# Optimization experiments

Hardware: AMD Instinct MI355X
Metric: run time of the kernel (lower is better)

The kernel has to match this reference:

```python
import jax, jax.numpy as jnp
import numpy as np

B, H, Q, D = 2, 8, 4096, 32
GH, GW = 32, 32  # key grid height/width


def setup_inputs() -> dict:
    key = jax.random.key(0)
    k1, k2, k3, k4 = jax.random.split(key, 4)
    queries = jax.random.normal(k1, (B, H, Q, D), dtype=jnp.float32)
    keys = jax.random.normal(k2, (B, H, GH, GW, D), dtype=jnp.float32)
    pos = jax.random.randint(k3, (B, Q, 2), 0, GH)  # integer (y, x) grid position of each query
    rel_bias = jax.random.normal(k4, (H, 2 * GH - 1, 2 * GW - 1), dtype=jnp.float32)
    return {"queries": queries, "keys": keys, "pos": pos, "rel_bias": rel_bias}


def reference(queries, keys, pos, rel_bias):
    # queries: [B,H,Q,D]; keys: [B,H,GH,GW,D]; pos: [B,Q,2] int; rel_bias: [H,2GH-1,2GW-1]
    b, h, q, d = queries.shape
    gh, gw = keys.shape[2], keys.shape[3]
    scale = 1.0 / jnp.sqrt(jnp.asarray(d, queries.dtype))
    # attention scores against every grid cell: [B,H,Q,GH,GW]
    scores = jnp.einsum('bhqd,bhijd->bhqij', queries, keys) * scale
    # relative offset indices into the bias table
    rel_y = jnp.arange(gh)[None, None, :] - pos[..., 0][..., None] + (gh - 1)  # [B,Q,GH]
    rel_x = jnp.arange(gw)[None, None, :] - pos[..., 1][..., None] + (gw - 1)  # [B,Q,GW]
    # gather per-head bias: [H,B,Q,GH,GW] -> [B,H,Q,GH,GW]
    bias = rel_bias[:, rel_y[:, :, :, None], rel_x[:, :, None, :]]
    bias = jnp.transpose(bias, (1, 0, 2, 3, 4))
    logits = scores + bias
    attn = jax.nn.softmax(logits.reshape(b, h, q, gh * gw), axis=-1)
    return attn.reshape(b, h, q, gh, gw)
```

## Files before the change

### kernel.cpp

```cpp
#include <hip/hip_runtime.h>

namespace {
constexpr int B_ = 2, H_ = 8, Q_ = 4096, D_ = 32;
constexpr int NPOS = 1024;
constexpr int NB = 63;
constexpr int NT = 512;
constexpr int QCHUNK = 128;
constexpr float SCALE = 0.17677669529663687f;
constexpr float LOG2E = 1.4426950408889634f;
constexpr float C1 = SCALE * LOG2E;
}

typedef __attribute__((ext_vector_type(8))) short short8;
typedef __attribute__((ext_vector_type(4))) float float4v;

__device__ __forceinline__ unsigned short f2bf(float f) {
  unsigned u = __float_as_uint(f);
  u += 0x7fffu + ((u >> 16) & 1u);
  return (unsigned short)(u >> 16);
}

__device__ __forceinline__ float fexp2(float x) {
#if defined(__has_builtin)
#if __has_builtin(__builtin_amdgcn_exp2f)
  return __builtin_amdgcn_exp2f(x);
#else
  return exp2f(x);
#endif
#else
  return exp2f(x);
#endif
}

__device__ __forceinline__ float frcp(float x) {
#if defined(__has_builtin)
#if __has_builtin(__builtin_amdgcn_rcpf)
  return __builtin_amdgcn_rcpf(x);
#else
  return 1.0f / x;
#endif
#else
  return 1.0f / x;
#endif
}

__global__ __launch_bounds__(NT, 4)
void rga_kernel(const float* __restrict__ queries,
                const float* __restrict__ keys,
                const int*   __restrict__ pos,
                const float* __restrict__ rel_bias,
                float* __restrict__ out) {
  __shared__ __align__(16) unsigned short klds[NPOS * D_];

  const int t    = threadIdx.x;
  const int lane = t & 63;
  const int w    = t >> 6;
  const int m    = lane & 15;
  const int quad = lane >> 4;
  const int h  = blockIdx.y;
  const int b  = blockIdx.z;
  const int bh = b * H_ + h;
  const int q0 = blockIdx.x * QCHUNK;

  {
    const float4* src = (const float4*)(keys + (size_t)bh * (NPOS * D_));
    #pragma unroll
    for (int i = 0; i < (NPOS * D_ / 4) / NT; ++i) {
      float4 v = src[i * NT + t];
      unsigned lo = (unsigned)f2bf(v.x) | ((unsigned)f2bf(v.y) << 16);
      unsigned hi = (unsigned)f2bf(v.z) | ((unsigned)f2bf(v.w) << 16);
      ((uint2*)klds)[i * NT + t] = make_uint2(lo, hi);
    }
  }
  __syncthreads();

  const int qrow = q0 + w * 16 + m;

  short8 afrag;
  {
    const float* qp = queries + ((size_t)(bh * Q_) + qrow) * D_ + quad * 8;
    float4 x = *(const float4*)(qp);
    float4 y = *(const float4*)(qp + 4);
    afrag[0] = (short)f2bf(x.x); afrag[1] = (short)f2bf(x.y);
    afrag[2] = (short)f2bf(x.z); afrag[3] = (short)f2bf(x.w);
    afrag[4] = (short)f2bf(y.x); afrag[5] = (short)f2bf(y.y);
    afrag[6] = (short)f2bf(y.z); afrag[7] = (short)f2bf(y.w);
  }

  const float* bbase;
  {
    int2 p = *(const int2*)(pos + ((size_t)b * Q_ + qrow) * 2);
    bbase = rel_bias + (size_t)h * (NB * NB)
          + (31 - p.x) * NB + (31 - p.y) + quad * 4;
  }

  const unsigned short* kbase = klds + m * D_ + quad * 8;

  float sum = 0.f;
  #pragma unroll
  for (int n = 0; n < NPOS / 16; ++n) {
    const short8 kf = *(const short8*)(kbase + n * 512);
    float4v acc = __builtin_amdgcn_mfma_f32_16x16x32_bf16(
        kf, afrag, (float4v){0.f, 0.f, 0.f, 0.f}, 0, 0, 0);
    float4v bv;
    __builtin_memcpy(&bv, bbase + (n >> 1) * NB + ((n & 1) << 4), 16);
    float e0 = fexp2(acc[0] * C1 + bv[0] * LOG2E);
    float e1 = fexp2(acc[1] * C1 + bv[1] * LOG2E);
    float e2 = fexp2(acc[2] * C1 + bv[2] * LOG2E);
    float e3 = fexp2(acc[3] * C1 + bv[3] * LOG2E);
    sum += (e0 + e1) + (e2 + e3);
  }
  sum += __shfl_xor(sum, 16, 64);
  sum += __shfl_xor(sum, 32, 64);
  const float rinv = frcp(sum);

  float* orow = out + ((size_t)(bh * Q_) + qrow) * NPOS + quad * 4;
  #pragma unroll
  for (int n = 0; n < NPOS / 16; ++n) {
    const short8 kf = *(const short8*)(kbase + n * 512);
    float4v acc = __builtin_amdgcn_mfma_f32_16x16x32_bf16(
        kf, afrag, (float4v){0.f, 0.f, 0.f, 0.f}, 0, 0, 0);
    float4v bv;
    __builtin_memcpy(&bv, bbase + (n >> 1) * NB + ((n & 1) << 4), 16);
    float4v ev;
    ev[0] = fexp2(acc[0] * C1 + bv[0] * LOG2E) * rinv;
    ev[1] = fexp2(acc[1] * C1 + bv[1] * LOG2E) * rinv;
    ev[2] = fexp2(acc[2] * C1 + bv[2] * LOG2E) * rinv;
    ev[3] = fexp2(acc[3] * C1 + bv[3] * LOG2E) * rinv;
    __builtin_nontemporal_store(ev, (float4v*)(orow + n * 16));
  }
}

extern "C" void kernel_launch(void* const* d_in, const int* in_sizes, int n_in,
                              void* d_out, int out_size, void* d_ws, size_t ws_size,
                              hipStream_t stream) {
  const float* queries  = (const float*)d_in[0];
  const float* keys     = (const float*)d_in[1];
  const int*   pos      = (const int*)d_in[2];
  const float* rel_bias = (const float*)d_in[3];
  float* out = (float*)d_out;

  dim3 grid(Q_ / QCHUNK, H_, B_);
  dim3 block(NT);
  hipLaunchKernelGGL(rga_kernel, grid, block, 0, stream,
                     queries, keys, pos, rel_bias, out);
}
```

Before: 339.5 us.

## Split key columns across waves, cache exps as bf16 in registers, swizzle LDS

Each block now covers 64 queries with 16 waves. Every group of 4 waves splits the 1024 key positions so that each wave handles 256 columns, and the partial row sums are combined through shared memory. The exponentials from the first pass are kept in registers as truncated bf16 pairs. The second pass only rescales and stores them instead of redoing the MFMA, the bias loads and exp2. The key LDS layout gets an XOR swizzle so reads avoid bank conflicts. The cost is an extra block barrier, fewer queries per block for the same key staging work, and a loss of output precision from truncating to bf16.

```diff
diff --git a/kernel.cpp b/kernel.cpp
--- a/kernel.cpp
+++ b/kernel.cpp
@@ -4,8 +4,8 @@
 constexpr int B_ = 2, H_ = 8, Q_ = 4096, D_ = 32;
 constexpr int NPOS = 1024;
 constexpr int NB = 63;
-constexpr int NT = 512;
-constexpr int QCHUNK = 128;
+constexpr int NT = 1024;
+constexpr int QCHUNK = 64;
 constexpr float SCALE = 0.17677669529663687f;
 constexpr float LOG2E = 1.4426950408889634f;
 constexpr float C1 = SCALE * LOG2E;
@@ -18,6 +18,10 @@
   unsigned u = __float_as_uint(f);
   u += 0x7fffu + ((u >> 16) & 1u);
   return (unsigned short)(u >> 16);
+}
+
+__device__ __forceinline__ unsigned pack2bf(float a, float b) {
+  return (unsigned)f2bf(a) | ((unsigned)f2bf(b) << 16);
 }
 
 __device__ __forceinline__ float fexp2(float x) {
@@ -44,37 +48,59 @@
 #endif
 }
 
+__device__ __forceinline__ unsigned pack_hi16(unsigned hi_from, unsigned lo_from) {
+#if defined(__has_builtin)
+#if __has_builtin(__builtin_amdgcn_perm)
+  return __builtin_amdgcn_perm(hi_from, lo_from, 0x07060302u);
+#else
+  return (lo_from >> 16) | (hi_from & 0xffff0000u);
+#endif
+#else
+  return (lo_from >> 16) | (hi_from & 0xffff0000u);
+#endif
+}
+
 __global__ __launch_bounds__(NT, 4)
 void rga_kernel(const float* __restrict__ queries,
                 const float* __restrict__ keys,
                 const int*   __restrict__ pos,
                 const float* __restrict__ rel_bias,
                 float* __restrict__ out) {
-  __shared__ __align__(16) unsigned short klds[NPOS * D_];
+  __shared__ __align__(16) unsigned char klds[NPOS * 64];
 
   const int t    = threadIdx.x;
   const int lane = t & 63;
   const int w    = t >> 6;
   const int m    = lane & 15;
   const int quad = lane >> 4;
+  const int rg   = w >> 2;
+  const int cw   = w & 3;
   const int h  = blockIdx.y;
   const int b  = blockIdx.z;
   const int bh = b * H_ + h;
   const int q0 = blockIdx.x * QCHUNK;
 
   {
-    const float4* src = (const float4*)(keys + (size_t)bh * (NPOS * D_));
+    const float* src = keys + (size_t)bh * (NPOS * D_);
     #pragma unroll
-    for (int i = 0; i < (NPOS * D_ / 4) / NT; ++i) {
-      float4 v = src[i * NT + t];
-      unsigned lo = (unsigned)f2bf(v.x) | ((unsigned)f2bf(v.y) << 16);
-      unsigned hi = (unsigned)f2bf(v.z) | ((unsigned)f2bf(v.w) << 16);
-      ((uint2*)klds)[i * NT + t] = make_uint2(lo, hi);
+    for (int i = 0; i < 4; ++i) {
+      const int c = i * NT + t;
+      const int p = c >> 2;
+      const int cq = c & 3;
+      float4 x = *(const float4*)(src + (size_t)c * 8);
+      float4 y = *(const float4*)(src + (size_t)c * 8 + 4);
+      uint4 v;
+      v.x = pack2bf(x.x, x.y);
+      v.y = pack2bf(x.z, x.w);
+      v.z = pack2bf(y.x, y.y);
+      v.w = pack2bf(y.z, y.w);
+      const int pq = cq ^ (p & 3) ^ ((p >> 2) & 3);
+      *(uint4*)(klds + (size_t)p * 64 + pq * 16) = v;
     }
   }
   __syncthreads();
 
-  const int qrow = q0 + w * 16 + m;
+  const int qrow = q0 + rg * 16 + m;
 
   short8 afrag;
   {
@@ -94,12 +120,15 @@
           + (31 - p.x) * NB + (31 - p.y) + quad * 4;
   }
 
-  const unsigned short* kbase = klds + m * D_ + quad * 8;
+  const unsigned char* kbase =
+      klds + (size_t)m * 64 + ((quad ^ (m & 3) ^ ((m >> 2) & 3)) << 4);
 
   float sum = 0.f;
+  unsigned Epk[32];
   #pragma unroll
-  for (int n = 0; n < NPOS / 16; ++n) {
-    const short8 kf = *(const short8*)(kbase + n * 512);
+  for (int k = 0; k < 16; ++k) {
+    const int n = cw * 16 + k;
+    const short8 kf = *(const short8*)(kbase + n * 1024);
     float4v acc = __builtin_amdgcn_mfma_f32_16x16x32_bf16(
         kf, afrag, (float4v){0.f, 0.f, 0.f, 0.f}, 0, 0, 0);
     float4v bv;
@@ -109,24 +138,31 @@
     float e2 = fexp2(acc[2] * C1 + bv[2] * LOG2E);
     float e3 = fexp2(acc[3] * C1 + bv[3] * LOG2E);
     sum += (e0 + e1) + (e2 + e3);
+    Epk[2 * k]     = pack_hi16(__float_as_uint(e1), __float_as_uint(e0));
+    Epk[2 * k + 1] = pack_hi16(__float_as_uint(e3), __float_as_uint(e2));
   }
+
   sum += __shfl_xor(sum, 16, 64);
   sum += __shfl_xor(sum, 32, 64);
-  const float rinv = frcp(sum);
+
+  __syncthreads();
+  float* slds = (float*)klds;
+  if (lane < 16) slds[w * 16 + m] = sum;
+  __syncthreads();
+  const float full = (slds[rg * 64 + m]      + slds[rg * 64 + 16 + m]) +
+                     (slds[rg * 64 + 32 + m] + slds[rg * 64 + 48 + m]);
+  const float rinv = frcp(full);
 
   float* orow = out + ((size_t)(bh * Q_) + qrow) * NPOS + quad * 4;
   #pragma unroll
-  for (int n = 0; n < NPOS / 16; ++n) {
-    const short8 kf = *(const short8*)(kbase + n * 512);
-    float4v acc = __builtin_amdgcn_mfma_f32_16x16x32_bf16(
-        kf, afrag, (float4v){0.f, 0.f, 0.f, 0.f}, 0, 0, 0);
-    float4v bv;
-    __builtin_memcpy(&bv, bbase + (n >> 1) * NB + ((n & 1) << 4), 16);
+  for (int k = 0; k < 16; ++k) {
+    const int n = cw * 16 + k;
+    const unsigned ua = Epk[2 * k], ub = Epk[2 * k + 1];
     float4v ev;
-    ev[0] = fexp2(acc[0] * C1 + bv[0] * LOG2E) * rinv;
-    ev[1] = fexp2(acc[1] * C1 + bv[1] * LOG2E) * rinv;
-    ev[2] = fexp2(acc[2] * C1 + bv[2] * LOG2E) * rinv;
-    ev[3] = fexp2(acc[3] * C1 + bv[3] * LOG2E) * rinv;
+    ev[0] = __uint_as_float(ua << 16)          * rinv;
+    ev[1] = __uint_as_float(ua & 0xffff0000u)  * rinv;
+    ev[2] = __uint_as_float(ub << 16)          * rinv;
+    ev[3] = __uint_as_float(ub & 0xffff0000u)  * rinv;
     __builtin_nontemporal_store(ev, (float4v*)(orow + n * 16));
   }
 }
```

Result: faster. 331.1 us (-2.5%).

## Pre-pack keys to bf16 fragments and stage scores in LDS per row tile

Applied to the files above, without the earlier changes.

Adds a prep kernel that converts keys to bf16 once, in MFMA fragment order, into workspace. The main kernel now processes 16-row tiles. Each wave computes part of the key columns with one MFMA each and writes the scores to swizzled LDS, then each wave runs softmax over whole rows with fully coalesced 1KB row stores. This removes the duplicated MFMA/exp pass and the per-block LDS key conversion, and it makes the output writes contiguous per row. In exchange it adds an extra launch, two barriers per tile, and a 64KB LDS buffer that may limit occupancy.

```diff
diff --git a/kernel.cpp b/kernel.cpp
--- a/kernel.cpp
+++ b/kernel.cpp
@@ -5,7 +5,9 @@
 constexpr int NPOS = 1024;
 constexpr int NB = 63;
 constexpr int NT = 512;
-constexpr int QCHUNK = 128;
+constexpr int ROWTILE = 16;
+constexpr int TILES_PER_BLOCK = 8;
+constexpr int QCHUNK = ROWTILE * TILES_PER_BLOCK;
 constexpr float SCALE = 0.17677669529663687f;
 constexpr float LOG2E = 1.4426950408889634f;
 constexpr float C1 = SCALE * LOG2E;
@@ -18,6 +20,10 @@
   unsigned u = __float_as_uint(f);
   u += 0x7fffu + ((u >> 16) & 1u);
   return (unsigned short)(u >> 16);
+}
+
+__device__ __forceinline__ unsigned pack2bf(float a, float b) {
+  return (unsigned)f2bf(a) | ((unsigned)f2bf(b) << 16);
 }
 
 __device__ __forceinline__ float fexp2(float x) {
@@ -44,13 +50,30 @@
 #endif
 }
 
+__global__ __launch_bounds__(64)
+void rga_prep(const float* __restrict__ keys, unsigned short* __restrict__ kws) {
+  const int bid = blockIdx.x;
+  const int t   = threadIdx.x;
+  const int m = t & 15, q = t >> 4;
+  const int bh = bid >> 6, n = bid & 63;
+  const float* src = keys + ((size_t)bh * NPOS + n * 16 + m) * D_ + q * 8;
+  float4 x = *(const float4*)src;
+  float4 y = *(const float4*)(src + 4);
+  uint4 v;
+  v.x = pack2bf(x.x, x.y);
+  v.y = pack2bf(x.z, x.w);
+  v.z = pack2bf(y.x, y.y);
+  v.w = pack2bf(y.z, y.w);
+  *(uint4*)(kws + ((size_t)bid * 64 + t) * 8) = v;
+}
+
 __global__ __launch_bounds__(NT, 4)
-void rga_kernel(const float* __restrict__ queries,
-                const float* __restrict__ keys,
-                const int*   __restrict__ pos,
-                const float* __restrict__ rel_bias,
-                float* __restrict__ out) {
-  __shared__ __align__(16) unsigned short klds[NPOS * D_];
+void rga_main(const float* __restrict__ queries,
+              const unsigned short* __restrict__ kws,
+              const int*   __restrict__ pos,
+              const float* __restrict__ rel_bias,
+              float* __restrict__ out) {
+  __shared__ __align__(16) float slds[ROWTILE * NPOS];
 
   const int t    = threadIdx.x;
   const int lane = t & 63;
@@ -62,72 +85,74 @@
   const int bh = b * H_ + h;
   const int q0 = blockIdx.x * QCHUNK;
 
-  {
-    const float4* src = (const float4*)(keys + (size_t)bh * (NPOS * D_));
+  const unsigned short* kbh = kws + (size_t)bh * (64 * 64 * 8);
+  const float* bias_h = rel_bias + (size_t)h * (NB * NB);
+
+  for (int tile = 0; tile < TILES_PER_BLOCK; ++tile) {
+    const int qt0 = q0 + tile * ROWTILE;
+
+    short8 afrag;
+    {
+      const float* qp = queries + ((size_t)(bh * Q_) + qt0 + m) * D_ + quad * 8;
+      float4 x = *(const float4*)(qp);
+      float4 y = *(const float4*)(qp + 4);
+      afrag[0] = (short)f2bf(x.x); afrag[1] = (short)f2bf(x.y);
+      afrag[2] = (short)f2bf(x.z); afrag[3] = (short)f2bf(x.w);
+      afrag[4] = (short)f2bf(y.x); afrag[5] = (short)f2bf(y.y);
+      afrag[6] = (short)f2bf(y.z); afrag[7] = (short)f2bf(y.w);
+    }
     #pragma unroll
-    for (int i = 0; i < (NPOS * D_ / 4) / NT; ++i) {
-      float4 v = src[i * NT + t];
-      unsigned lo = (unsigned)f2bf(v.x) | ((unsigned)f2bf(v.y) << 16);
-      unsigned hi = (unsigned)f2bf(v.z) | ((unsigned)f2bf(v.w) << 16);
-      ((uint2*)klds)[i * NT + t] = make_uint2(lo, hi);
+    for (int k = 0; k < 8; ++k) {
+      const int n = w * 8 + k;
+      const short8 kf = *(const short8*)(kbh + ((size_t)n * 64 + lane) * 8);
+      float4v acc = __builtin_amdgcn_mfma_f32_16x16x32_bf16(
+          kf, afrag, (float4v){0.f, 0.f, 0.f, 0.f}, 0, 0, 0);
+      const int off = (n * 64 + quad * 16) ^ (m << 4);
+      *(float4v*)((char*)slds + m * 4096 + off) = acc;
     }
-  }
-  __syncthreads();
+    __syncthreads();
 
-  const int qrow = q0 + w * 16 + m;
+    #pragma unroll
+    for (int rr = 0; rr < 2; ++rr) {
+      const int lr   = w * 2 + rr;
+      const int qrow = qt0 + lr;
+      int2 p = *(const int2*)(pos + ((size_t)b * Q_ + qrow) * 2);
+      const float* brow = bias_h + (31 - p.x) * NB + (31 - p.y);
+      const int ioff = (lane >> 3) * NB + (lane & 7) * 4;
 
-  short8 afrag;
-  {
-    const float* qp = queries + ((size_t)(bh * Q_) + qrow) * D_ + quad * 8;
-    float4 x = *(const float4*)(qp);
-    float4 y = *(const float4*)(qp + 4);
-    afrag[0] = (short)f2bf(x.x); afrag[1] = (short)f2bf(x.y);
-    afrag[2] = (short)f2bf(x.z); afrag[3] = (short)f2bf(x.w);
-    afrag[4] = (short)f2bf(y.x); afrag[5] = (short)f2bf(y.y);
-    afrag[6] = (short)f2bf(y.z); afrag[7] = (short)f2bf(y.w);
-  }
+      float e[16];
+      float sum = 0.f;
+      #pragma unroll
+      for (int n2 = 0; n2 < 4; ++n2) {
+        const int off = (n2 * 1024 + lane * 16) ^ (lr << 4);
+        float4v s4 = *(const float4v*)((char*)slds + lr * 4096 + off);
+        float4v bv;
+        __builtin_memcpy(&bv, brow + n2 * 8 * NB + ioff, 16);
+        float e0 = fexp2(s4[0] * C1 + bv[0] * LOG2E);
+        float e1 = fexp2(s4[1] * C1 + bv[1] * LOG2E);
+        float e2 = fexp2(s4[2] * C1 + bv[2] * LOG2E);
+        float e3 = fexp2(s4[3] * C1 + bv[3] * LOG2E);
+        e[n2 * 4 + 0] = e0; e[n2 * 4 + 1] = e1;
+        e[n2 * 4 + 2] = e2; e[n2 * 4 + 3] = e3;
+        sum += (e0 + e1) + (e2 + e3);
+      }
+      #pragma unroll
+      for (int mask = 1; mask <= 32; mask <<= 1)
+        sum += __shfl_xor(sum, mask, 64);
+      const float rinv = frcp(sum);
 
-  const float* bbase;
-  {
-    int2 p = *(const int2*)(pos + ((size_t)b * Q_ + qrow) * 2);
-    bbase = rel_bias + (size_t)h * (NB * NB)
-          + (31 - p.x) * NB + (31 - p.y) + quad * 4;
-  }
-
-  const unsigned short* kbase = klds + m * D_ + quad * 8;
-
-  float sum = 0.f;
-  #pragma unroll
-  for (int n = 0; n < NPOS / 16; ++n) {
-    const short8 kf = *(const short8*)(kbase + n * 512);
-    float4v acc = __builtin_amdgcn_mfma_f32_16x16x32_bf16(
-        kf, afrag, (float4v){0.f, 0.f, 0.f, 0.f}, 0, 0, 0);
-    float4v bv;
-    __builtin_memcpy(&bv, bbase + (n >> 1) * NB + ((n & 1) << 4), 16);
-    float e0 = fexp2(acc[0] * C1 + bv[0] * LOG2E);
-    float e1 = fexp2(acc[1] * C1 + bv[1] * LOG2E);
-    float e2 = fexp2(acc[2] * C1 + bv[2] * LOG2E);
-    float e3 = fexp2(acc[3] * C1 + bv[3] * LOG2E);
-    sum += (e0 + e1) + (e2 + e3);
-  }
-  sum += __shfl_xor(sum, 16, 64);
-  sum += __shfl_xor(sum, 32, 64);
-  const float rinv = frcp(sum);
-
-  float* orow = out + ((size_t)(bh * Q_) + qrow) * NPOS + quad * 4;
-  #pragma unroll
-  for (int n = 0; n < NPOS / 16; ++n) {
-    const short8 kf = *(const short8*)(kbase + n * 512);
-    float4v acc = __builtin_amdgcn_mfma_f32_16x16x32_bf16(
-        kf, afrag, (float4v){0.f, 0.f, 0.f, 0.f}, 0, 0, 0);
-    float4v bv;
-    __builtin_memcpy(&bv, bbase + (n >> 1) * NB + ((n & 1) << 4), 16);
-    float4v ev;
-    ev[0] = fexp2(acc[0] * C1 + bv[0] * LOG2E) * rinv;
-    ev[1] = fexp2(acc[1] * C1 + bv[1] * LOG2E) * rinv;
-    ev[2] = fexp2(acc[2] * C1 + bv[2] * LOG2E) * rinv;
-    ev[3] = fexp2(acc[3] * C1 + bv[3] * LOG2E) * rinv;
-    __builtin_nontemporal_store(ev, (float4v*)(orow + n * 16));
+      float* orow = out + ((size_t)(bh * Q_) + qrow) * NPOS;
+      #pragma unroll
+      for (int n2 = 0; n2 < 4; ++n2) {
+        float4v ev;
+        ev[0] = e[n2 * 4 + 0] * rinv;
+        ev[1] = e[n2 * 4 + 1] * rinv;
+        ev[2] = e[n2 * 4 + 2] * rinv;
+        ev[3] = e[n2 * 4 + 3] * rinv;
+        __builtin_nontemporal_store(ev, (float4v*)(orow + n2 * 256 + lane * 4));
+      }
+    }
+    __syncthreads();
   }
 }
 
@@ -139,9 +164,12 @@
   const int*   pos      = (const int*)d_in[2];
   const float* rel_bias = (const float*)d_in[3];
   float* out = (float*)d_out;
+  unsigned short* kws = (unsigned short*)d_ws;
 
+  hipLaunchKernelGGL(rga_prep, dim3(B_ * H_ * 64), dim3(64), 0, stream,
+                     keys, kws);
   dim3 grid(Q_ / QCHUNK, H_, B_);
   dim3 block(NT);
-  hipLaunchKernelGGL(rga_kernel, grid, block, 0, stream,
-                     queries, keys, pos, rel_bias, out);
+  hipLaunchKernelGGL(rga_main, grid, block, 0, stream,
+                     queries, kws, pos, rel_bias, out);
 }
```

Measured after the change: 291.9 us. 1.16x faster.
